# Kernel optimization log

Hardware: AMD Instinct MI355X
Metric: run time of the kernel (lower is better)

## Reference

```python
import jax, jax.numpy as jnp
import numpy as np

N, D, H, C, K, L = 50000, 256, 128, 40, 4, 2
E = 800000


def setup_inputs() -> dict:
    key = jax.random.key(0)
    ks = jax.random.split(key, 20)
    g = lambda k, s: jax.random.normal(k, s, dtype=jnp.float32) * 0.05
    z = lambda s: jnp.zeros(s, dtype=jnp.float32)
    return {
        "x": jax.random.normal(ks[0], (N, D), dtype=jnp.float32),
        "edge_index": jax.random.randint(ks[1], (2, E), 0, N, dtype=jnp.int32),
        "fc0_w": g(ks[2], (D, H)), "fc0_b": z((H,)),
        "fc1_w": g(ks[3], (H, C)), "fc1_b": z((C,)),
        "env_w": g(ks[4], (L, H, K)), "env_b": z((L, K)),
        "conv_w": g(ks[5], (L, K, 2 * H, H)),
        "q_w": g(ks[6], (H, H)), "q_b": z((H,)),
        "k_w": g(ks[7], (H, H)), "k_b": z((H,)),
        "v_w": g(ks[8], (H, H)), "v_b": z((H,)),
        "envp_w": g(ks[9], (H, K)), "envp_b": z((K,)),
        "genv_w": g(ks[10], (K, H, H)),
        "gt_w": g(ks[11], (H, H)), "gt_b": z((H,)),
    }


def _gcn_conv(h, row, col, n):
    # symmetric normalization using in-degree array (deg computed from col, as in source)
    deg = jax.ops.segment_sum(jnp.ones_like(col, dtype=h.dtype), col, num_segments=n)
    inv = jnp.where(deg > 0, 1.0 / jnp.sqrt(deg), 0.0)
    val = inv[col] * inv[row]                      # [E]
    msg = val[:, None] * h[row]                    # [E, H] gather
    return jax.ops.segment_sum(msg, col, num_segments=n)  # scatter to dst


def _canet_conv(h, row, col, env, w):
    # sum_k e_k [W_D^k * A_norm h ; W_S^k * h] via cat + per-env GEMM, residual
    hi = jnp.concatenate([_gcn_conv(h, row, col, h.shape[0]), h], axis=1)  # [N, 2H]
    out_k = jnp.einsum('nd,kdh->nkh', hi, w)       # [N, K, H]
    return jnp.einsum('nk,nkh->nh', env, out_k) + h


def _linear_transformer(h, q_w, q_b, k_w, k_b, v_w, v_b, envp_w, envp_b):
    n = h.shape[0]
    q = h @ q_w + q_b
    k = h @ k_w + k_b
    v = h @ v_w + v_b
    q = q / jnp.maximum(jnp.linalg.norm(q), 1e-12)  # fro-norm of whole matrix
    k = k / jnp.maximum(jnp.linalg.norm(k), 1e-12)
    ksum = jnp.sum(k, axis=0)                       # k^T @ ones -> [H]
    attn_norm = 1.0 + (q @ ksum)[:, None] / n       # [N,1]
    gr = (v + q @ (k.T @ v) / n) / jnp.maximum(attn_norm, 1e-12)
    return gr, gr @ envp_w + envp_b


def _forward(x, edge_index, fc0_w, fc0_b, fc1_w, fc1_b, env_w, env_b, conv_w,
             q_w, q_b, k_w, k_b, v_w, v_b, envp_w, envp_b, genv_w, gt_w, gt_b):
    row, col = edge_index[0], edge_index[1]
    h = jax.nn.relu(x @ fc0_w + fc0_b)
    for i in range(L):
        logits = h @ env_w[i] + env_b[i]            # node env encoder
        env = jax.nn.softmax(logits, axis=-1)       # eval-mode sampling
        h = jax.nn.relu(_canet_conv(h, row, col, env, conv_w[i]))
    local_logits = h @ fc1_w + fc1_b                # [N, C]
    gr, glog = _linear_transformer(h, q_w, q_b, k_w, k_b, v_w, v_b, envp_w, envp_b)
    genv = jax.nn.softmax(glog, axis=-1)            # [N, K]
    gpe = jnp.einsum('nh,khe->nke', gr, genv_w)     # per-env global transforms
    ctx = jnp.einsum('nk,nkh->nh', genv, gpe)
    gh = jax.nn.relu(ctx @ gt_w + gt_b)
    global_logits = gh @ fc1_w + fc1_b
    return 0.5 * (local_logits + global_logits)     # fused prediction


def reference(x, edge_index, fc0_w, fc0_b, fc1_w, fc1_b, env_w, env_b, conv_w,
              q_w, q_b, k_w, k_b, v_w, v_b, envp_w, envp_b, genv_w, gt_w, gt_b):
    return _forward(x, edge_index, fc0_w, fc0_b, fc1_w, fc1_b, env_w, env_b, conv_w,
                    q_w, q_b, k_w, k_b, v_w, v_b, envp_w, envp_b, genv_w, gt_w, gt_b)
```

## Files before the change

kernel.cpp:

```cpp
#include <hip/hip_runtime.h>

#define DEV __device__ __forceinline__

static constexpr int NN = 50000;
static constexpr int DD = 256;
static constexpr int HH = 128;
static constexpr int CC = 40;
static constexpr int KK = 4;
static constexpr int EE = 800000;
static constexpr int MP = 50176;
static constexpr int SKV = 196;
static constexpr int CPB = 8;
static constexpr int CSB = 391;
static constexpr int MBC = 391;

typedef __attribute__((ext_vector_type(8))) short bf16x8;
typedef __attribute__((ext_vector_type(4))) float f32x4;

DEV unsigned short f2bf(float f) {
  union { float f; unsigned int i; } c; c.f = f;
  unsigned int x = c.i;
  x += 0x7FFFu + ((x >> 16) & 1u);
  return (unsigned short)(x >> 16);
}
DEV float bfbits2f(unsigned int hi16bits) {
  union { unsigned int i; float f; } c; c.i = hi16bits; return c.f;
}

__global__ void MLEI_12970801234193_kernel(float* out, int n) {
  int i = blockIdx.x * blockDim.x + threadIdx.x;
  if (i < n) out[i] = 7.0f;
}

DEV void tc(const float* __restrict__ src, unsigned short* __restrict__ dst,
            int i, int K, int N) {
  int m = i / (K * N);
  int rem = i - m * K * N;
  int k = rem / N;
  int n = rem - k * N;
  dst[(size_t)m * K * N + (size_t)n * K + k] = f2bf(src[i]);
}

__global__ __launch_bounds__(256) void prep_kernel(
    int* __restrict__ deg, unsigned short* __restrict__ kT, unsigned short* __restrict__ vT,
    const float* __restrict__ fc0_w, unsigned short* __restrict__ Btfc0,
    const float* __restrict__ q_w, unsigned short* __restrict__ Btq,
    const float* __restrict__ k_w, unsigned short* __restrict__ Btk,
    const float* __restrict__ v_w, unsigned short* __restrict__ Btv,
    const float* __restrict__ gt_w, unsigned short* __restrict__ Btgt,
    const float* __restrict__ fc1_w, unsigned short* __restrict__ Btfc1,
    const float* __restrict__ conv_w, unsigned short* __restrict__ Btconv,
    const float* __restrict__ genv_w, unsigned short* __restrict__ Btgenv) {
  int i = blockIdx.x * 256 + threadIdx.x;
  if (i < NN) { deg[i] = 0; return; }
  i -= NN;
  const int PW = MP - NN;
  if (i < HH * PW) {
    int f = i / PW, c = i - f * PW;
    kT[(size_t)f * MP + NN + c] = 0;
    vT[(size_t)f * MP + NN + c] = 0;
    return;
  }
  i -= HH * PW;
  if (i < 32768) { tc(fc0_w, Btfc0, i, 256, 128); return; }
  i -= 32768;
  if (i < 16384) { tc(q_w, Btq, i, 128, 128); return; }
  i -= 16384;
  if (i < 16384) { tc(k_w, Btk, i, 128, 128); return; }
  i -= 16384;
  if (i < 16384) { tc(v_w, Btv, i, 128, 128); return; }
  i -= 16384;
  if (i < 16384) { tc(gt_w, Btgt, i, 128, 128); return; }
  i -= 16384;
  if (i < 5120) { tc(fc1_w, Btfc1, i, 128, 40); return; }
  i -= 5120;
  if (i < 262144) { tc(conv_w, Btconv, i, 256, 128); return; }
  i -= 262144;
  if (i < 65536) { tc(genv_w, Btgenv, i, 128, 128); }
}

__global__ __launch_bounds__(256) void mgemm_kernel(
    const float* __restrict__ A, const float* __restrict__ Aadd, int lda,
    const unsigned short* __restrict__ Bt, int K,
    int emode, float* __restrict__ out, int ldo,
    const float* __restrict__ bias, const float* __restrict__ resid, int ldr,
    const float* __restrict__ anorm, const float* __restrict__ red,
    unsigned short* __restrict__ outT,
    unsigned short* __restrict__ outBf, const float* __restrict__ rowscale,
    int M, int Nd) {
  __shared__ unsigned short As[2][128][40];
  __shared__ unsigned short Bs[2][128][40];
  const int tid = threadIdx.x, lane = tid & 63, wave = tid >> 6;
  const int quad = lane >> 4, l16 = lane & 15;
  const int wm = (wave >> 1) * 64, wn = (wave & 1) * 64;
  const int bm = blockIdx.x * 128;
  const int srow = tid >> 1, skh = (tid & 1) * 16;
  const int grow = bm + srow;
  const bool rowok = grow < M;
  const bool colok = srow < Nd;
  const int NCH = K >> 5;

  f32x4 acc[4][4];
#pragma unroll
  for (int i = 0; i < 4; ++i)
#pragma unroll
    for (int j = 0; j < 4; ++j)
#pragma unroll
      for (int r = 0; r < 4; ++r) acc[i][j][r] = 0.f;

  float vaA[16], vaB[16];
  bf16x8 bA0, bA1, bB0, bB1;

  auto LOAD = [&](int kc, float (&va)[16], bf16x8& b0, bf16x8& b1) {
    int k0 = kc << 5;
    if (rowok) {
      const float* ap = A + (size_t)grow * lda + k0 + skh;
      float4 v0 = *(const float4*)(ap + 0), v1 = *(const float4*)(ap + 4);
      float4 v2 = *(const float4*)(ap + 8), v3 = *(const float4*)(ap + 12);
      va[0] = v0.x; va[1] = v0.y; va[2] = v0.z; va[3] = v0.w;
      va[4] = v1.x; va[5] = v1.y; va[6] = v1.z; va[7] = v1.w;
      va[8] = v2.x; va[9] = v2.y; va[10] = v2.z; va[11] = v2.w;
      va[12] = v3.x; va[13] = v3.y; va[14] = v3.z; va[15] = v3.w;
      if (Aadd) {
        const float* ap2 = Aadd + (size_t)grow * lda + k0 + skh;
        float4 w0 = *(const float4*)(ap2 + 0), w1 = *(const float4*)(ap2 + 4);
        float4 w2 = *(const float4*)(ap2 + 8), w3 = *(const float4*)(ap2 + 12);
        va[0] += w0.x; va[1] += w0.y; va[2] += w0.z; va[3] += w0.w;
        va[4] += w1.x; va[5] += w1.y; va[6] += w1.z; va[7] += w1.w;
        va[8] += w2.x; va[9] += w2.y; va[10] += w2.z; va[11] += w2.w;
        va[12] += w3.x; va[13] += w3.y; va[14] += w3.z; va[15] += w3.w;
      }
    }
    if (colok) {
      const unsigned short* bp = Bt + (size_t)srow * K + k0 + skh;
      b0 = *(const bf16x8*)(bp);
      b1 = *(const bf16x8*)(bp + 8);
    } else {
#pragma unroll
      for (int z = 0; z < 8; ++z) { b0[z] = 0; b1[z] = 0; }
    }
  };

  auto STORE = [&](int buf, const float (&va)[16], const bf16x8& b0, const bf16x8& b1) {
    bf16x8 p0, p1;
    if (rowok) {
#pragma unroll
      for (int z = 0; z < 8; ++z) { p0[z] = (short)f2bf(va[z]); p1[z] = (short)f2bf(va[z + 8]); }
    } else {
#pragma unroll
      for (int z = 0; z < 8; ++z) { p0[z] = 0; p1[z] = 0; }
    }
    *(bf16x8*)&As[buf][srow][skh] = p0;
    *(bf16x8*)&As[buf][srow][skh + 8] = p1;
    *(bf16x8*)&Bs[buf][srow][skh] = b0;
    *(bf16x8*)&Bs[buf][srow][skh + 8] = b1;
  };

  auto MFMA = [&](int buf) {
    bf16x8 af[4], bfr[4];
#pragma unroll
    for (int i = 0; i < 4; ++i) af[i] = *(const bf16x8*)&As[buf][wm + i * 16 + l16][quad * 8];
#pragma unroll
    for (int j = 0; j < 4; ++j) bfr[j] = *(const bf16x8*)&Bs[buf][wn + j * 16 + l16][quad * 8];
#pragma unroll
    for (int i = 0; i < 4; ++i)
#pragma unroll
      for (int j = 0; j < 4; ++j)
        acc[i][j] = __builtin_amdgcn_mfma_f32_16x16x32_bf16(af[i], bfr[j], acc[i][j], 0, 0, 0);
  };

  LOAD(0, vaA, bA0, bA1);
  if (NCH > 1) LOAD(1, vaB, bB0, bB1);
  STORE(0, vaA, bA0, bA1);
  __syncthreads();

  for (int kc = 0; kc < NCH; kc += 2) {
    if (kc + 2 < NCH) LOAD(kc + 2, vaA, bA0, bA1);
    MFMA(0);
    if (kc + 1 < NCH) STORE(1, vaB, bB0, bB1);
    __syncthreads();
    if (kc + 1 < NCH) {
      if (kc + 3 < NCH) LOAD(kc + 3, vaB, bB0, bB1);
      MFMA(1);
      if (kc + 2 < NCH) STORE(0, vaA, bA0, bA1);
      __syncthreads();
    }
  }

  float s2 = (emode == 3) ? red[2] : 0.f;
#pragma unroll
  for (int j = 0; j < 4; ++j) {
    int col = wn + j * 16 + l16;
    if (col >= Nd) continue;
    float bv = bias ? bias[col] : 0.f;
#pragma unroll
    for (int i = 0; i < 4; ++i) {
      int row0 = bm + wm + i * 16 + quad * 4;
      if (row0 >= M) continue;
      float o[4];
#pragma unroll
      for (int r = 0; r < 4; ++r) {
        float a = acc[i][j][r];
        int row = row0 + r;
        if (emode == 0) o[r] = a + bv;
        else if (emode == 1) o[r] = fmaxf(a + bv, 0.f);
        else if (emode == 3) o[r] = (resid[(size_t)row * ldr + col] + a * s2) / anorm[row];
        else o[r] = 0.5f * a + bv;
        out[(size_t)row * ldo + col] = o[r];
      }
      if (outT) {
        ushort4 pk;
        pk.x = f2bf(o[0]); pk.y = f2bf(o[1]); pk.z = f2bf(o[2]); pk.w = f2bf(o[3]);
        *(ushort4*)&outT[(size_t)col * MP + row0] = pk;
      }
      if (outBf) {
#pragma unroll
        for (int r = 0; r < 4; ++r) {
          float rs = rowscale ? rowscale[row0 + r] : 1.f;
          outBf[(size_t)(row0 + r) * 128 + col] = f2bf(o[r] * rs);
        }
      }
    }
  }
}

__global__ __launch_bounds__(256) void mgemm_qkv_kernel(
    const float* __restrict__ A,
    const unsigned short* __restrict__ Btq, const unsigned short* __restrict__ Btk,
    const unsigned short* __restrict__ Btv,
    const float* __restrict__ q_b, const float* __restrict__ k_b,
    const float* __restrict__ v_b,
    float* __restrict__ outq, float* __restrict__ outk, float* __restrict__ outv,
    unsigned short* __restrict__ kT, unsigned short* __restrict__ vT, int M) {
  __shared__ unsigned short As[2][128][40];
  __shared__ unsigned short Bs[2][128][40];
  const int which = blockIdx.x % 3;
  const int bx = blockIdx.x / 3;
  const unsigned short* Bt = (which == 0) ? Btq : (which == 1) ? Btk : Btv;
  const float* bias = (which == 0) ? q_b : (which == 1) ? k_b : v_b;
  float* out = (which == 0) ? outq : (which == 1) ? outk : outv;
  unsigned short* outT = (which == 0) ? nullptr : (which == 1) ? kT : vT;

  const int tid = threadIdx.x, lane = tid & 63, wave = tid >> 6;
  const int quad = lane >> 4, l16 = lane & 15;
  const int wm = (wave >> 1) * 64, wn = (wave & 1) * 64;
  const int bm = bx * 128;
  const int srow = tid >> 1, skh = (tid & 1) * 16;
  const int grow = bm + srow;
  const bool rowok = grow < M;
  const int NCH = 4;

  f32x4 acc[4][4];
#pragma unroll
  for (int i = 0; i < 4; ++i)
#pragma unroll
    for (int j = 0; j < 4; ++j)
#pragma unroll
      for (int r = 0; r < 4; ++r) acc[i][j][r] = 0.f;

  float vaA[16], vaB[16];
  bf16x8 bA0, bA1, bB0, bB1;

  auto LOAD = [&](int kc, float (&va)[16], bf16x8& b0, bf16x8& b1) {
    int k0 = kc << 5;
    if (rowok) {
      const float* ap = A + (size_t)grow * 128 + k0 + skh;
      float4 v0 = *(const float4*)(ap + 0), v1 = *(const float4*)(ap + 4);
      float4 v2 = *(const float4*)(ap + 8), v3 = *(const float4*)(ap + 12);
      va[0] = v0.x; va[1] = v0.y; va[2] = v0.z; va[3] = v0.w;
      va[4] = v1.x; va[5] = v1.y; va[6] = v1.z; va[7] = v1.w;
      va[8] = v2.x; va[9] = v2.y; va[10] = v2.z; va[11] = v2.w;
      va[12] = v3.x; va[13] = v3.y; va[14] = v3.z; va[15] = v3.w;
    }
    const unsigned short* bp = Bt + (size_t)srow * 128 + k0 + skh;
    b0 = *(const bf16x8*)(bp);
    b1 = *(const bf16x8*)(bp + 8);
  };

  auto STORE = [&](int buf, const float (&va)[16], const bf16x8& b0, const bf16x8& b1) {
    bf16x8 p0, p1;
    if (rowok) {
#pragma unroll
      for (int z = 0; z < 8; ++z) { p0[z] = (short)f2bf(va[z]); p1[z] = (short)f2bf(va[z + 8]); }
    } else {
#pragma unroll
      for (int z = 0; z < 8; ++z) { p0[z] = 0; p1[z] = 0; }
    }
    *(bf16x8*)&As[buf][srow][skh] = p0;
    *(bf16x8*)&As[buf][srow][skh + 8] = p1;
    *(bf16x8*)&Bs[buf][srow][skh] = b0;
    *(bf16x8*)&Bs[buf][srow][skh + 8] = b1;
  };

  auto MFMA = [&](int buf) {
    bf16x8 af[4], bfr[4];
#pragma unroll
    for (int i = 0; i < 4; ++i) af[i] = *(const bf16x8*)&As[buf][wm + i * 16 + l16][quad * 8];
#pragma unroll
    for (int j = 0; j < 4; ++j) bfr[j] = *(const bf16x8*)&Bs[buf][wn + j * 16 + l16][quad * 8];
#pragma unroll
    for (int i = 0; i < 4; ++i)
#pragma unroll
      for (int j = 0; j < 4; ++j)
        acc[i][j] = __builtin_amdgcn_mfma_f32_16x16x32_bf16(af[i], bfr[j], acc[i][j], 0, 0, 0);
  };

  LOAD(0, vaA, bA0, bA1);
  LOAD(1, vaB, bB0, bB1);
  STORE(0, vaA, bA0, bA1);
  __syncthreads();

  for (int kc = 0; kc < NCH; kc += 2) {
    if (kc + 2 < NCH) LOAD(kc + 2, vaA, bA0, bA1);
    MFMA(0);
    if (kc + 1 < NCH) STORE(1, vaB, bB0, bB1);
    __syncthreads();
    if (kc + 1 < NCH) {
      if (kc + 3 < NCH) LOAD(kc + 3, vaB, bB0, bB1);
      MFMA(1);
      if (kc + 2 < NCH) STORE(0, vaA, bA0, bA1);
      __syncthreads();
    }
  }

#pragma unroll
  for (int j = 0; j < 4; ++j) {
    int col = wn + j * 16 + l16;
    float bv = bias[col];
#pragma unroll
    for (int i = 0; i < 4; ++i) {
      int row0 = bm + wm + i * 16 + quad * 4;
      if (row0 >= M) continue;
      float o[4];
#pragma unroll
      for (int r = 0; r < 4; ++r) {
        o[r] = acc[i][j][r] + bv;
        out[(size_t)(row0 + r) * 128 + col] = o[r];
      }
      if (outT) {
        ushort4 pk;
        pk.x = f2bf(o[0]); pk.y = f2bf(o[1]); pk.z = f2bf(o[2]); pk.w = f2bf(o[3]);
        *(ushort4*)&outT[(size_t)col * MP + row0] = pk;
      }
    }
  }
}

__global__ __launch_bounds__(256) void colstats_ktv_kernel(
    const unsigned short* __restrict__ kT, const unsigned short* __restrict__ vT,
    float* __restrict__ part,
    const float* __restrict__ q, const float* __restrict__ k,
    float* __restrict__ partK, float* __restrict__ partS, int n) {
  __shared__ unsigned short As[2][128][40];
  __shared__ unsigned short Bs[2][128][40];
  const int tid = threadIdx.x;

  if (blockIdx.x < SKV) {
    const int lane = tid & 63, wave = tid >> 6;
    const int quad = lane >> 4, l16 = lane & 15;
    const int wm = (wave >> 1) * 64, wn = (wave & 1) * 64;
    const int srow = tid >> 1, skh = (tid & 1) * 16;

    f32x4 acc[4][4];
#pragma unroll
    for (int i = 0; i < 4; ++i)
#pragma unroll
      for (int j = 0; j < 4; ++j)
#pragma unroll
        for (int r = 0; r < 4; ++r) acc[i][j][r] = 0.f;

    const int nb0 = blockIdx.x * (CPB * 32);
    bf16x8 kA0, kA1, vA0, vA1, kB0, kB1, vB0, vB1;

    auto LOAD = [&](int c, bf16x8& k0, bf16x8& k1, bf16x8& v0, bf16x8& v1) {
      int nb = nb0 + c * 32;
      const unsigned short* kp = kT + (size_t)srow * MP + nb + skh;
      k0 = *(const bf16x8*)(kp);
      k1 = *(const bf16x8*)(kp + 8);
      const unsigned short* vp = vT + (size_t)srow * MP + nb + skh;
      v0 = *(const bf16x8*)(vp);
      v1 = *(const bf16x8*)(vp + 8);
    };
    auto STORE = [&](int buf, const bf16x8& k0, const bf16x8& k1, const bf16x8& v0, const bf16x8& v1) {
      *(bf16x8*)&As[buf][srow][skh] = k0;
      *(bf16x8*)&As[buf][srow][skh + 8] = k1;
      *(bf16x8*)&Bs[buf][srow][skh] = v0;
      *(bf16x8*)&Bs[buf][srow][skh + 8] = v1;
    };
    auto MFMA = [&](int buf) {
      bf16x8 af[4], bfr[4];
#pragma unroll
      for (int i = 0; i < 4; ++i) af[i] = *(const bf16x8*)&As[buf][wm + i * 16 + l16][quad * 8];
#pragma unroll
      for (int j = 0; j < 4; ++j) bfr[j] = *(const bf16x8*)&Bs[buf][wn + j * 16 + l16][quad * 8];
#pragma unroll
      for (int i = 0; i < 4; ++i)
#pragma unroll
        for (int j = 0; j < 4; ++j)
          acc[i][j] = __builtin_amdgcn_mfma_f32_16x16x32_bf16(af[i], bfr[j], acc[i][j], 0, 0, 0);
    };

    LOAD(0, kA0, kA1, vA0, vA1);
    LOAD(1, kB0, kB1, vB0, vB1);
    STORE(0, kA0, kA1, vA0, vA1);
    __syncthreads();

    for (int c = 0; c < CPB; c += 2) {
      if (c + 2 < CPB) LOAD(c + 2, kA0, kA1, vA0, vA1);
      MFMA(0);
      if (c + 1 < CPB) STORE(1, kB0, kB1, vB0, vB1);
      __syncthreads();
      if (c + 1 < CPB) {
        if (c + 3 < CPB) LOAD(c + 3, kB0, kB1, vB0, vB1);
        MFMA(1);
        if (c + 2 < CPB) STORE(0, kA0, kA1, vA0, vA1);
        __syncthreads();
      }
    }

    float* pb = part + (size_t)blockIdx.x * 16384;
#pragma unroll
    for (int j = 0; j < 4; ++j) {
      int col = wn + j * 16 + l16;
#pragma unroll
      for (int i = 0; i < 4; ++i) {
        int row0 = wm + i * 16 + quad * 4;
        *(f32x4*)&pb[col * 128 + row0] = acc[i][j];
      }
    }
  } else {
    const int bid = blockIdx.x - SKV;
    float* sks = (float*)&As[0][0][0];
    float* ssq = sks + 256;
    float* ssk = ssq + 256;
    int ty = tid >> 7, tx = tid & 127;
    int lo = bid * 128 + ty, hi = min(n, bid * 128 + 128);
    float ks = 0.f, sq = 0.f, sk = 0.f;
    for (int r = lo; r < hi; r += 2) {
      float kv = k[(size_t)r * HH + tx];
      float qv = q[(size_t)r * HH + tx];
      ks += kv; sq += qv * qv; sk += kv * kv;
    }
    sks[ty * 128 + tx] = ks; ssq[tid] = sq; ssk[tid] = sk;
    __syncthreads();
    if (ty == 0) partK[(size_t)bid * 128 + tx] = sks[tx] + sks[128 + tx];
    for (int off = 128; off > 0; off >>= 1) {
      if (tid < off) { ssq[tid] += ssq[tid + off]; ssk[tid] += ssk[tid + off]; }
      __syncthreads();
    }
    if (tid == 0) { partS[bid * 2] = ssq[0]; partS[bid * 2 + 1] = ssk[0]; }
  }
}

__global__ void ktv_reduce_kernel(const float* __restrict__ part,
                                  unsigned short* __restrict__ Btktv) {
  int i = blockIdx.x * blockDim.x + threadIdx.x;
  if (i >= 16384) return;
  float s0 = 0.f, s1 = 0.f, s2 = 0.f, s3 = 0.f;
  int b = 0;
  for (; b + 3 < SKV; b += 4) {
    s0 += part[(size_t)b * 16384 + i];
    s1 += part[(size_t)(b + 1) * 16384 + i];
    s2 += part[(size_t)(b + 2) * 16384 + i];
    s3 += part[(size_t)(b + 3) * 16384 + i];
  }
  for (; b < SKV; ++b) s0 += part[(size_t)b * 16384 + i];
  Btktv[i] = f2bf((s0 + s1) + (s2 + s3));
}

__global__ __launch_bounds__(256) void mconv_kernel(
    const float* __restrict__ A1, const float* __restrict__ A2,
    const float* __restrict__ env, const unsigned short* __restrict__ Btc, int Kpe,
    int relu_resid, const float* __restrict__ resid, float* __restrict__ out,
    unsigned short* __restrict__ outBf, const float* __restrict__ rowscale, int M) {
  __shared__ unsigned short As[2][128][40];
  __shared__ unsigned short Bs[2][128][40];
  const int tid = threadIdx.x, lane = tid & 63, wave = tid >> 6;
  const int quad = lane >> 4, l16 = lane & 15;
  const int wm = (wave >> 1) * 64, wn = (wave & 1) * 64;
  const int bm = blockIdx.x * 128;
  const int srow = tid >> 1, skh = (tid & 1) * 16;
  const int grow = bm + srow;
  const bool rowok = grow < M;

  float ev0 = 0.f, ev1 = 0.f, ev2 = 0.f, ev3 = 0.f;
  if (rowok) {
    float4 e4 = *(const float4*)&env[(size_t)grow * 4];
    ev0 = e4.x; ev1 = e4.y; ev2 = e4.z; ev3 = e4.w;
  }

  const int npe = Kpe >> 5;
  const int NPH = npe << 2;

  f32x4 acc[4][4];
#pragma unroll
  for (int i = 0; i < 4; ++i)
#pragma unroll
    for (int j = 0; j < 4; ++j)
#pragma unroll
      for (int r = 0; r < 4; ++r) acc[i][j][r] = 0.f;

  float aC[16], aN[16];
  bf16x8 b0, b1;

  auto LOADA = [&](int kc, float (&dst)[16]) {
    int kof = kc << 5;
    const float* Asrc = A1;
    int ks = kof;
    if (A2 && kof >= 128) { Asrc = A2; ks = kof - 128; }
    if (rowok) {
      const float* ap = Asrc + (size_t)grow * 128 + ks + skh;
      float4 v0 = *(const float4*)(ap + 0), v1 = *(const float4*)(ap + 4);
      float4 v2 = *(const float4*)(ap + 8), v3 = *(const float4*)(ap + 12);
      dst[0] = v0.x; dst[1] = v0.y; dst[2] = v0.z; dst[3] = v0.w;
      dst[4] = v1.x; dst[5] = v1.y; dst[6] = v1.z; dst[7] = v1.w;
      dst[8] = v2.x; dst[9] = v2.y; dst[10] = v2.z; dst[11] = v2.w;
      dst[12] = v3.x; dst[13] = v3.y; dst[14] = v3.z; dst[15] = v3.w;
    }
  };

  auto LOADB = [&](int e, int kc) {
    const unsigned short* bp = Btc + ((size_t)e * 128 + srow) * Kpe + (kc << 5) + skh;
    b0 = *(const bf16x8*)(bp);
    b1 = *(const bf16x8*)(bp + 8);
  };

  auto STORE = [&](int buf, const float (&a)[16], float ev) {
    bf16x8 p0, p1;
    if (rowok) {
#pragma unroll
      for (int z = 0; z < 8; ++z) {
        p0[z] = (short)f2bf(a[z] * ev);
        p1[z] = (short)f2bf(a[z + 8] * ev);
      }
    } else {
#pragma unroll
      for (int z = 0; z < 8; ++z) { p0[z] = 0; p1[z] = 0; }
    }
    *(bf16x8*)&As[buf][srow][skh] = p0;
    *(bf16x8*)&As[buf][srow][skh + 8] = p1;
    *(bf16x8*)&Bs[buf][srow][skh] = b0;
    *(bf16x8*)&Bs[buf][srow][skh + 8] = b1;
  };

  auto MFMA = [&](int buf) {
    bf16x8 af[4], bfr[4];
#pragma unroll
    for (int i = 0; i < 4; ++i) af[i] = *(const bf16x8*)&As[buf][wm + i * 16 + l16][quad * 8];
#pragma unroll
    for (int j = 0; j < 4; ++j) bfr[j] = *(const bf16x8*)&Bs[buf][wn + j * 16 + l16][quad * 8];
#pragma unroll
    for (int i = 0; i < 4; ++i)
#pragma unroll
      for (int j = 0; j < 4; ++j)
        acc[i][j] = __builtin_amdgcn_mfma_f32_16x16x32_bf16(af[i], bfr[j], acc[i][j], 0, 0, 0);
  };

  LOADA(0, aC);
  LOADB(0, 0);
  if (npe > 1) LOADA(1, aN);
  STORE(0, aC, ev0);
  __syncthreads();

  for (int kc = 0; kc < npe; ++kc) {
#pragma unroll
    for (int e = 0; e < 4; ++e) {
      const int p = (kc << 2) + e;
      const int cur = e & 1;
      const bool more = (p + 1) < NPH;
      if (more) {
        LOADB((e + 1) & 3, kc + (e == 3 ? 1 : 0));
      }
      MFMA(cur);
      if (more) {
        if (e == 3) {
#pragma unroll
          for (int z = 0; z < 16; ++z) aC[z] = aN[z];
        }
        float evn = (e == 0) ? ev1 : (e == 1) ? ev2 : (e == 2) ? ev3 : ev0;
        STORE(cur ^ 1, aC, evn);
        if (e == 3 && kc + 2 < npe) LOADA(kc + 2, aN);
      }
      __syncthreads();
    }
  }

#pragma unroll
  for (int j = 0; j < 4; ++j) {
    int col = wn + j * 16 + l16;
#pragma unroll
    for (int i = 0; i < 4; ++i) {
      int row0 = bm + wm + i * 16 + quad * 4;
      if (row0 >= M) continue;
#pragma unroll
      for (int r = 0; r < 4; ++r) {
        int row = row0 + r;
        float a = acc[i][j][r];
        float o = relu_resid ? fmaxf(a + resid[(size_t)row * 128 + col], 0.f) : a;
        out[(size_t)row * 128 + col] = o;
        if (outBf) {
          float rs = rowscale ? rowscale[row] : 1.f;
          outBf[(size_t)row * 128 + col] = f2bf(o * rs);
        }
      }
    }
  }
}

__global__ void count_kernel(const int* ei, int* deg, int E) {
  int e = blockIdx.x * blockDim.x + threadIdx.x;
  if (e >= E) return;
  atomicAdd(&deg[ei[E + e]], 1);
}

__global__ __launch_bounds__(128) void scan1_kernel(const int* __restrict__ deg,
                                                    int* __restrict__ bsum, int n) {
  __shared__ int sh[128];
  int t = threadIdx.x;
  int i = blockIdx.x * 128 + t;
  sh[t] = (i < n) ? deg[i] : 0;
  __syncthreads();
  for (int off = 64; off > 0; off >>= 1) {
    if (t < off) sh[t] += sh[t + off];
    __syncthreads();
  }
  if (t == 0) bsum[blockIdx.x] = sh[0];
}

__global__ __launch_bounds__(512) void scan2_kernel(const int* __restrict__ bsum,
                                                    int* __restrict__ boff, int nb,
                                                    int* __restrict__ startN) {
  __shared__ int sh[512];
  int t = threadIdx.x;
  int v0 = (t < nb) ? bsum[t] : 0;
  sh[t] = v0;
  __syncthreads();
  for (int off = 1; off < 512; off <<= 1) {
    int v = sh[t];
    int add = (t >= off) ? sh[t - off] : 0;
    __syncthreads();
    sh[t] = v + add;
    __syncthreads();
  }
  if (t < nb) boff[t] = sh[t] - v0;
  if (t == nb - 1) *startN = sh[t];
}

__global__ __launch_bounds__(128) void scan3_kernel(const int* __restrict__ deg,
                                                    const int* __restrict__ boff,
                                                    int* __restrict__ start,
                                                    int* __restrict__ cursor,
                                                    float* __restrict__ inv, int n) {
  __shared__ int sh[128];
  int t = threadIdx.x;
  int i = blockIdx.x * 128 + t;
  int d = (i < n) ? deg[i] : 0;
  sh[t] = d;
  __syncthreads();
  for (int off = 1; off < 128; off <<= 1) {
    int v = sh[t];
    int add = (t >= off) ? sh[t - off] : 0;
    __syncthreads();
    sh[t] = v + add;
    __syncthreads();
  }
  if (i < n) {
    int p = boff[blockIdx.x] + sh[t] - d;
    start[i] = p; cursor[i] = p;
    inv[i] = (d > 0) ? rsqrtf((float)d) : 0.f;
  }
}

__global__ void fill_kernel(const int* ei, int* cursor, int* bucket, int E) {
  int e = blockIdx.x * blockDim.x + threadIdx.x;
  if (e >= E) return;
  int r = ei[e], c = ei[E + e];
  int pos = atomicAdd(&cursor[c], 1);
  bucket[pos] = r;
}

__global__ __launch_bounds__(256) void gather_env_kernel(
    const unsigned short* __restrict__ hs, const int* __restrict__ start,
    const int* __restrict__ bucket, const float* __restrict__ inv,
    const float* __restrict__ h, const float* __restrict__ w,
    const float* __restrict__ b,
    float* __restrict__ agg, float* __restrict__ env, int n) {
  int node = blockIdx.x * 4 + (threadIdx.x >> 6);
  if (node >= n) return;
  const int lane = threadIdx.x & 63;
  const int half = lane >> 5, l32 = lane & 31;
  const int f4 = l32 * 4;

  float2 hv = *(const float2*)&h[(size_t)node * 128 + 2 * lane];
  float4 w0 = *(const float4*)&w[(size_t)(2 * lane) * 4];
  float4 w1 = *(const float4*)&w[(size_t)(2 * lane + 1) * 4];
  float p0 = hv.x * w0.x + hv.y * w1.x;
  float p1 = hv.x * w0.y + hv.y * w1.y;
  float p2 = hv.x * w0.z + hv.y * w1.z;
  float p3 = hv.x * w0.w + hv.y * w1.w;

  int s0 = start[node], s1 = start[node + 1];
  float a0 = 0.f, a1 = 0.f, a2 = 0.f, a3 = 0.f;
  int j = s0 + half;
  for (; j + 2 < s1; j += 4) {
    int r0 = bucket[j], r1 = bucket[j + 2];
    uint2 u0 = *(const uint2*)&hs[(size_t)r0 * 128 + f4];
    uint2 u1 = *(const uint2*)&hs[(size_t)r1 * 128 + f4];
    a0 += bfbits2f(u0.x << 16); a1 += bfbits2f(u0.x & 0xFFFF0000u);
    a2 += bfbits2f(u0.y << 16); a3 += bfbits2f(u0.y & 0xFFFF0000u);
    a0 += bfbits2f(u1.x << 16); a1 += bfbits2f(u1.x & 0xFFFF0000u);
    a2 += bfbits2f(u1.y << 16); a3 += bfbits2f(u1.y & 0xFFFF0000u);
  }
  for (; j < s1; j += 2) {
    int r = bucket[j];
    uint2 u = *(const uint2*)&hs[(size_t)r * 128 + f4];
    a0 += bfbits2f(u.x << 16); a1 += bfbits2f(u.x & 0xFFFF0000u);
    a2 += bfbits2f(u.y << 16); a3 += bfbits2f(u.y & 0xFFFF0000u);
  }

#pragma unroll
  for (int s = 1; s <= 32; s <<= 1) {
    p0 += __shfl_xor(p0, s);
    p1 += __shfl_xor(p1, s);
    p2 += __shfl_xor(p2, s);
    p3 += __shfl_xor(p3, s);
  }

  a0 += __shfl_xor(a0, 32);
  a1 += __shfl_xor(a1, 32);
  a2 += __shfl_xor(a2, 32);
  a3 += __shfl_xor(a3, 32);
  if (half == 0) {
    float iv = inv[node];
    *(float4*)&agg[(size_t)node * 128 + f4] = make_float4(iv * a0, iv * a1, iv * a2, iv * a3);
  }
  if (lane == 0) {
    float l0 = p0 + b[0], l1 = p1 + b[1], l2 = p2 + b[2], l3 = p3 + b[3];
    float m = fmaxf(fmaxf(l0, l1), fmaxf(l2, l3));
    float e0 = __expf(l0 - m), e1 = __expf(l1 - m), e2 = __expf(l2 - m), e3 = __expf(l3 - m);
    float s = 1.f / (e0 + e1 + e2 + e3);
    *(float4*)&env[(size_t)node * 4] = make_float4(e0 * s, e1 * s, e2 * s, e3 * s);
  }
}

__global__ __launch_bounds__(256) void env_softmax_kernel(const float* __restrict__ h,
                                                          const float* __restrict__ w,
                                                          const float* __restrict__ b,
                                                          float* __restrict__ env, int M) {
  __shared__ float hsd[64][129];
  __shared__ float ws[HH * KK];
  int tid = threadIdx.x;
  int base = blockIdx.x * 64;
  for (int i = tid; i < HH * KK; i += 256) ws[i] = w[i];
  {
    int row = tid >> 2, q4 = (tid & 3) * 32;
    int g = base + row;
    if (g < M) {
      const float* hp = h + (size_t)g * HH + q4;
#pragma unroll
      for (int z = 0; z < 8; ++z) {
        float4 v = *(const float4*)(hp + z * 4);
        hsd[row][q4 + z * 4 + 0] = v.x; hsd[row][q4 + z * 4 + 1] = v.y;
        hsd[row][q4 + z * 4 + 2] = v.z; hsd[row][q4 + z * 4 + 3] = v.w;
      }
    }
  }
  __syncthreads();
  if (tid < 64 && base + tid < M) {
    float l0 = b[0], l1 = b[1], l2 = b[2], l3 = b[3];
    for (int d = 0; d < HH; ++d) {
      float hv = hsd[tid][d];
      l0 += hv * ws[d * 4 + 0]; l1 += hv * ws[d * 4 + 1];
      l2 += hv * ws[d * 4 + 2]; l3 += hv * ws[d * 4 + 3];
    }
    float m = fmaxf(fmaxf(l0, l1), fmaxf(l2, l3));
    float e0 = __expf(l0 - m), e1 = __expf(l1 - m), e2 = __expf(l2 - m), e3 = __expf(l3 - m);
    float s = 1.f / (e0 + e1 + e2 + e3);
    *(float4*)(env + (size_t)(base + tid) * KK) = make_float4(e0 * s, e1 * s, e2 * s, e3 * s);
  }
}

__global__ __launch_bounds__(256) void colstats2_kernel(
    const float* __restrict__ partK, const float* __restrict__ partS,
    float* __restrict__ ksum, float* __restrict__ red) {
  int t = threadIdx.x;
  if (t < 128) {
    float s = 0.f;
    for (int b = 0; b < CSB; ++b) s += partK[(size_t)b * 128 + t];
    ksum[t] = s;
  } else if (t == 128 || t == 129) {
    float s = 0.f;
    for (int b = 0; b < CSB; ++b) s += partS[b * 2 + (t - 128)];
    red[t - 128] = s;
  }
}

__global__ void scale_kernel(float* red, int n) {
  float nq = fmaxf(sqrtf(red[0]), 1e-12f);
  float nk = fmaxf(sqrtf(red[1]), 1e-12f);
  red[2] = 1.f / (nq * nk * (float)n);
}

__global__ __launch_bounds__(256) void anorm_kernel(const float* q, const float* ksum,
                                                    const float* red, float* anorm, int M) {
  __shared__ float ks[HH];
  for (int i = threadIdx.x; i < HH; i += blockDim.x) ks[i] = ksum[i];
  __syncthreads();
  int n = blockIdx.x * blockDim.x + threadIdx.x;
  if (n >= M) return;
  const float* qp = q + (size_t)n * HH;
  float d = 0.f;
  for (int i = 0; i < HH; ++i) d += qp[i] * ks[i];
  float a = 1.f + d * red[2];
  anorm[n] = fmaxf(a, 1e-12f);
}

extern "C" void kernel_launch(void* const* d_in, const int* in_sizes, int n_in,
                              void* d_out, int out_size, void* d_ws, size_t ws_size,
                              hipStream_t stream) {
  const float* x = (const float*)d_in[0];
  const int* ei = (const int*)d_in[1];
  const float* fc0_w = (const float*)d_in[2];
  const float* fc0_b = (const float*)d_in[3];
  const float* fc1_w = (const float*)d_in[4];
  const float* fc1_b = (const float*)d_in[5];
  const float* env_w = (const float*)d_in[6];
  const float* env_b = (const float*)d_in[7];
  const float* conv_w = (const float*)d_in[8];
  const float* q_w = (const float*)d_in[9];
  const float* q_b = (const float*)d_in[10];
  const float* k_w = (const float*)d_in[11];
  const float* k_b = (const float*)d_in[12];
  const float* v_w = (const float*)d_in[13];
  const float* v_b = (const float*)d_in[14];
  const float* envp_w = (const float*)d_in[15];
  const float* envp_b = (const float*)d_in[16];
  const float* genv_w = (const float*)d_in[17];
  const float* gt_w = (const float*)d_in[18];
  const float* gt_b = (const float*)d_in[19];
  float* out = (float*)d_out;

  const size_t NH = (size_t)NN * HH;
  float* W = (float*)d_ws;
  float* hA = W;
  float* hB = W + NH;
  float* agg = W + 2 * NH;
  float* vbuf = W + 3 * NH;
  float* gr = W + 4 * NH;
  float* env = W + 5 * NH;
  float* genv = env + (size_t)NN * KK;
  float* inv = genv + (size_t)NN * KK;
  float* anorm = inv + NN;
  float* ksum = anorm + NN;
  float* red = ksum + HH;
  int* deg = (int*)(red + 4);
  int* start = deg + NN;
  int* cursor = start + NN + 1;
  int* bucket = cursor + NN;
  int* bsum = bucket + EE;
  int* boff = bsum + CSB;
  unsigned short* wb = (unsigned short*)(((uintptr_t)(boff + CSB) + 15) & ~(uintptr_t)15);
  unsigned short* Btfc0 = wb;
  unsigned short* Btq = Btfc0 + 32768;
  unsigned short* Btk = Btq + 16384;
  unsigned short* Btv = Btk + 16384;
  unsigned short* Btgt = Btv + 16384;
  unsigned short* Btfc1 = Btgt + 16384;
  unsigned short* Btconv = Btfc1 + 5120;
  unsigned short* Btgenv = Btconv + 262144;
  unsigned short* Btktv = Btgenv + 65536;
  unsigned short* kTbf = Btktv + 16384;
  unsigned short* vTbf = kTbf + (size_t)HH * MP;
  unsigned short* hsb = vTbf + (size_t)HH * MP;
  float* part = (float*)(((uintptr_t)(hsb + NH) + 15) & ~(uintptr_t)15);
  float* partK = part + (size_t)SKV * 16384;
  float* partS = partK + (size_t)CSB * 128;

  float* q = agg;
  float* kb = hB;
  float* ctx = hB;
  float* gh = vbuf;

  dim3 b256(256);
  const int MB = MBC;
  const int PREP_TOT = NN + HH * (MP - NN) + 32768 + 4 * 16384 + 5120 + 262144 + 65536;

  prep_kernel<<<dim3((PREP_TOT + 255) / 256), b256, 0, stream>>>(
      deg, kTbf, vTbf, fc0_w, Btfc0, q_w, Btq, k_w, Btk, v_w, Btv,
      gt_w, Btgt, fc1_w, Btfc1, conv_w, Btconv, genv_w, Btgenv);

  count_kernel<<<dim3((EE + 255) / 256), b256, 0, stream>>>(ei, deg, EE);
  scan1_kernel<<<dim3(CSB), dim3(128), 0, stream>>>(deg, bsum, NN);
  scan2_kernel<<<dim3(1), dim3(512), 0, stream>>>(bsum, boff, CSB, start + NN);
  scan3_kernel<<<dim3(CSB), dim3(128), 0, stream>>>(deg, boff, start, cursor, inv, NN);
  fill_kernel<<<dim3((EE + 255) / 256), b256, 0, stream>>>(ei, cursor, bucket, EE);

  mgemm_kernel<<<dim3(MB), b256, 0, stream>>>(
      x, nullptr, DD, Btfc0, 256, 1, hA, HH, fc0_b, nullptr, 0, nullptr, nullptr,
      nullptr, hsb, inv, NN, HH);

  float* hcur = hA;
  float* hnext = hB;
  for (int l = 0; l < 2; ++l) {
    gather_env_kernel<<<dim3(NN / 4), b256, 0, stream>>>(
        hsb, start, bucket, inv, hcur, env_w + (size_t)l * HH * KK,
        env_b + (size_t)l * KK, agg, env, NN);
    mconv_kernel<<<dim3(MB), b256, 0, stream>>>(
        agg, hcur, env, Btconv + (size_t)l * 131072, 256, 1, hcur, hnext,
        (l == 0) ? hsb : nullptr, inv, NN);
    float* t = hcur; hcur = hnext; hnext = t;
  }

  mgemm_qkv_kernel<<<dim3(3 * MB), b256, 0, stream>>>(
      hcur, Btq, Btk, Btv, q_b, k_b, v_b, q, kb, vbuf, kTbf, vTbf, NN);

  colstats_ktv_kernel<<<dim3(SKV + CSB), b256, 0, stream>>>(
      kTbf, vTbf, part, q, kb, partK, partS, NN);
  colstats2_kernel<<<dim3(1), b256, 0, stream>>>(partK, partS, ksum, red);
  ktv_reduce_kernel<<<dim3(64), b256, 0, stream>>>(part, Btktv);
  scale_kernel<<<dim3(1), dim3(1), 0, stream>>>(red, NN);
  anorm_kernel<<<dim3((NN + 255) / 256), b256, 0, stream>>>(q, ksum, red, anorm, NN);

  mgemm_kernel<<<dim3(MB), b256, 0, stream>>>(
      q, nullptr, HH, Btktv, 128, 3, gr, HH, nullptr, vbuf, HH, anorm, red,
      nullptr, nullptr, nullptr, NN, HH);

  env_softmax_kernel<<<dim3((NN + 63) / 64), b256, 0, stream>>>(gr, envp_w, envp_b, genv, NN);

  mconv_kernel<<<dim3(MB), b256, 0, stream>>>(
      gr, nullptr, genv, Btgenv, 128, 0, nullptr, ctx, nullptr, nullptr, NN);

  mgemm_kernel<<<dim3(MB), b256, 0, stream>>>(
      ctx, nullptr, HH, Btgt, 128, 1, gh, HH, gt_b, nullptr, 0, nullptr, nullptr,
      nullptr, nullptr, nullptr, NN, HH);

  mgemm_kernel<<<dim3(MB), b256, 0, stream>>>(
      hcur, gh, HH, Btfc1, 128, 5, out, CC, fc1_b, nullptr, 0, nullptr, nullptr,
      nullptr, nullptr, nullptr, NN, CC);
}
```

Measured before the change: 657.3 us.

## Merge fc0 GEMM with CSR fill, fuse small reductions, widen gather loads

The fc0 GEMM and the edge-bucket fill kernel are merged into one launch, with different block ranges doing each job so they can run concurrently. The colstats2, ktv_reduce and scale kernels become a single reduce2 kernel, and the scale factor is recomputed inline wherever it is consumed. The neighbour gather now uses 16-byte loads with 16 lanes per row, covering four edges per iteration instead of two. Together these cut launch count and serial tiny kernels and raise memory-level parallelism in the gather, at the cost of more registers in the gather and a fused kernel that mixes heavy GEMM blocks with light atomic blocks.

```diff
diff --git a/kernel.cpp b/kernel.cpp
--- a/kernel.cpp
+++ b/kernel.cpp
@@ -13,6 +13,7 @@
 static constexpr int CPB = 8;
 static constexpr int CSB = 391;
 static constexpr int MBC = 391;
+static constexpr int FILLB = (EE + 255) / 256;
 
 typedef __attribute__((ext_vector_type(8))) short bf16x8;
 typedef __attribute__((ext_vector_type(4))) float f32x4;
@@ -79,7 +80,7 @@
   if (i < 65536) { tc(genv_w, Btgenv, i, 128, 128); }
 }
 
-__global__ __launch_bounds__(256) void mgemm_kernel(
+DEV void mgemm_body(
     const float* __restrict__ A, const float* __restrict__ Aadd, int lda,
     const unsigned short* __restrict__ Bt, int K,
     int emode, float* __restrict__ out, int ldo,
@@ -87,13 +88,13 @@
     const float* __restrict__ anorm, const float* __restrict__ red,
     unsigned short* __restrict__ outT,
     unsigned short* __restrict__ outBf, const float* __restrict__ rowscale,
-    int M, int Nd) {
+    int M, int Nd, int bx) {
   __shared__ unsigned short As[2][128][40];
   __shared__ unsigned short Bs[2][128][40];
   const int tid = threadIdx.x, lane = tid & 63, wave = tid >> 6;
   const int quad = lane >> 4, l16 = lane & 15;
   const int wm = (wave >> 1) * 64, wn = (wave & 1) * 64;
-  const int bm = blockIdx.x * 128;
+  const int bm = bx * 128;
   const int srow = tid >> 1, skh = (tid & 1) * 16;
   const int grow = bm + srow;
   const bool rowok = grow < M;
@@ -187,7 +188,12 @@
     }
   }
 
-  float s2 = (emode == 3) ? red[2] : 0.f;
+  float s2 = 0.f;
+  if (emode == 3) {
+    float nq = fmaxf(sqrtf(red[0]), 1e-12f);
+    float nk = fmaxf(sqrtf(red[1]), 1e-12f);
+    s2 = 1.f / (nq * nk * (float)M);
+  }
 #pragma unroll
   for (int j = 0; j < 4; ++j) {
     int col = wn + j * 16 + l16;
@@ -221,6 +227,36 @@
         }
       }
     }
+  }
+}
+
+__global__ __launch_bounds__(256) void mgemm_kernel(
+    const float* __restrict__ A, const float* __restrict__ Aadd, int lda,
+    const unsigned short* __restrict__ Bt, int K,
+    int emode, float* __restrict__ out, int ldo,
+    const float* __restrict__ bias, const float* __restrict__ resid, int ldr,
+    const float* __restrict__ anorm, const float* __restrict__ red,
+    unsigned short* __restrict__ outT,
+    unsigned short* __restrict__ outBf, const float* __restrict__ rowscale,
+    int M, int Nd) {
+  mgemm_body(A, Aadd, lda, Bt, K, emode, out, ldo, bias, resid, ldr, anorm, red,
+             outT, outBf, rowscale, M, Nd, blockIdx.x);
+}
+
+__global__ __launch_bounds__(256) void fc0_fill_kernel(
+    const float* __restrict__ x, const unsigned short* __restrict__ Btfc0,
+    const float* __restrict__ fc0_b, float* __restrict__ hA,
+    unsigned short* __restrict__ hsb, const float* __restrict__ inv,
+    const int* __restrict__ ei, int* __restrict__ cursor, int* __restrict__ bucket) {
+  if (blockIdx.x < MBC) {
+    mgemm_body(x, nullptr, DD, Btfc0, 256, 1, hA, HH, fc0_b, nullptr, 0, nullptr,
+               nullptr, nullptr, hsb, inv, NN, HH, blockIdx.x);
+  } else {
+    int e = (blockIdx.x - MBC) * 256 + threadIdx.x;
+    if (e >= EE) return;
+    int r = ei[e], c = ei[EE + e];
+    int pos = atomicAdd(&cursor[c], 1);
+    bucket[pos] = r;
   }
 }
 
@@ -452,20 +488,34 @@
   }
 }
 
-__global__ void ktv_reduce_kernel(const float* __restrict__ part,
-                                  unsigned short* __restrict__ Btktv) {
-  int i = blockIdx.x * blockDim.x + threadIdx.x;
-  if (i >= 16384) return;
-  float s0 = 0.f, s1 = 0.f, s2 = 0.f, s3 = 0.f;
-  int b = 0;
-  for (; b + 3 < SKV; b += 4) {
-    s0 += part[(size_t)b * 16384 + i];
-    s1 += part[(size_t)(b + 1) * 16384 + i];
-    s2 += part[(size_t)(b + 2) * 16384 + i];
-    s3 += part[(size_t)(b + 3) * 16384 + i];
-  }
-  for (; b < SKV; ++b) s0 += part[(size_t)b * 16384 + i];
-  Btktv[i] = f2bf((s0 + s1) + (s2 + s3));
+__global__ __launch_bounds__(256) void reduce2_kernel(
+    const float* __restrict__ partK, const float* __restrict__ partS,
+    float* __restrict__ ksum, float* __restrict__ red,
+    const float* __restrict__ part, unsigned short* __restrict__ Btktv) {
+  int t = threadIdx.x;
+  if (blockIdx.x == 0) {
+    if (t < 128) {
+      float s = 0.f;
+      for (int b = 0; b < CSB; ++b) s += partK[(size_t)b * 128 + t];
+      ksum[t] = s;
+    } else if (t == 128 || t == 129) {
+      float s = 0.f;
+      for (int b = 0; b < CSB; ++b) s += partS[b * 2 + (t - 128)];
+      red[t - 128] = s;
+    }
+  } else {
+    int i = (blockIdx.x - 1) * 256 + t;
+    float s0 = 0.f, s1 = 0.f, s2 = 0.f, s3 = 0.f;
+    int b = 0;
+    for (; b + 3 < SKV; b += 4) {
+      s0 += part[(size_t)b * 16384 + i];
+      s1 += part[(size_t)(b + 1) * 16384 + i];
+      s2 += part[(size_t)(b + 2) * 16384 + i];
+      s3 += part[(size_t)(b + 3) * 16384 + i];
+    }
+    for (; b < SKV; ++b) s0 += part[(size_t)b * 16384 + i];
+    Btktv[i] = f2bf((s0 + s1) + (s2 + s3));
+  }
 }
 
 __global__ __launch_bounds__(256) void mconv_kernel(
@@ -671,14 +721,6 @@
   }
 }
 
-__global__ void fill_kernel(const int* ei, int* cursor, int* bucket, int E) {
-  int e = blockIdx.x * blockDim.x + threadIdx.x;
-  if (e >= E) return;
-  int r = ei[e], c = ei[E + e];
-  int pos = atomicAdd(&cursor[c], 1);
-  bucket[pos] = r;
-}
-
 __global__ __launch_bounds__(256) void gather_env_kernel(
     const unsigned short* __restrict__ hs, const int* __restrict__ start,
     const int* __restrict__ bucket, const float* __restrict__ inv,
@@ -688,8 +730,8 @@
   int node = blockIdx.x * 4 + (threadIdx.x >> 6);
   if (node >= n) return;
   const int lane = threadIdx.x & 63;
-  const int half = lane >> 5, l32 = lane & 31;
-  const int f4 = l32 * 4;
+  const int quarter = lane >> 4, l16 = lane & 15;
+  const int f8 = l16 * 8;
 
   float2 hv = *(const float2*)&h[(size_t)node * 128 + 2 * lane];
   float4 w0 = *(const float4*)&w[(size_t)(2 * lane) * 4];
@@ -701,21 +743,28 @@
 
   int s0 = start[node], s1 = start[node + 1];
   float a0 = 0.f, a1 = 0.f, a2 = 0.f, a3 = 0.f;
-  int j = s0 + half;
-  for (; j + 2 < s1; j += 4) {
-    int r0 = bucket[j], r1 = bucket[j + 2];
-    uint2 u0 = *(const uint2*)&hs[(size_t)r0 * 128 + f4];
-    uint2 u1 = *(const uint2*)&hs[(size_t)r1 * 128 + f4];
+  float a4 = 0.f, a5 = 0.f, a6 = 0.f, a7 = 0.f;
+  int j = s0 + quarter;
+  for (; j + 4 < s1; j += 8) {
+    int r0 = bucket[j], r1 = bucket[j + 4];
+    uint4 u0 = *(const uint4*)&hs[(size_t)r0 * 128 + f8];
+    uint4 u1 = *(const uint4*)&hs[(size_t)r1 * 128 + f8];
     a0 += bfbits2f(u0.x << 16); a1 += bfbits2f(u0.x & 0xFFFF0000u);
     a2 += bfbits2f(u0.y << 16); a3 += bfbits2f(u0.y & 0xFFFF0000u);
+    a4 += bfbits2f(u0.z << 16); a5 += bfbits2f(u0.z & 0xFFFF0000u);
+    a6 += bfbits2f(u0.w << 16); a7 += bfbits2f(u0.w & 0xFFFF0000u);
     a0 += bfbits2f(u1.x << 16); a1 += bfbits2f(u1.x & 0xFFFF0000u);
     a2 += bfbits2f(u1.y << 16); a3 += bfbits2f(u1.y & 0xFFFF0000u);
-  }
-  for (; j < s1; j += 2) {
+    a4 += bfbits2f(u1.z << 16); a5 += bfbits2f(u1.z & 0xFFFF0000u);
+    a6 += bfbits2f(u1.w << 16); a7 += bfbits2f(u1.w & 0xFFFF0000u);
+  }
+  for (; j < s1; j += 4) {
     int r = bucket[j];
-    uint2 u = *(const uint2*)&hs[(size_t)r * 128 + f4];
+    uint4 u = *(const uint4*)&hs[(size_t)r * 128 + f8];
     a0 += bfbits2f(u.x << 16); a1 += bfbits2f(u.x & 0xFFFF0000u);
     a2 += bfbits2f(u.y << 16); a3 += bfbits2f(u.y & 0xFFFF0000u);
+    a4 += bfbits2f(u.z << 16); a5 += bfbits2f(u.z & 0xFFFF0000u);
+    a6 += bfbits2f(u.w << 16); a7 += bfbits2f(u.w & 0xFFFF0000u);
   }
 
 #pragma unroll
@@ -726,13 +775,19 @@
     p3 += __shfl_xor(p3, s);
   }
 
-  a0 += __shfl_xor(a0, 32);
-  a1 += __shfl_xor(a1, 32);
-  a2 += __shfl_xor(a2, 32);
-  a3 += __shfl_xor(a3, 32);
-  if (half == 0) {
+  a0 += __shfl_xor(a0, 16); a1 += __shfl_xor(a1, 16);
+  a2 += __shfl_xor(a2, 16); a3 += __shfl_xor(a3, 16);
+  a4 += __shfl_xor(a4, 16); a5 += __shfl_xor(a5, 16);
+  a6 += __shfl_xor(a6, 16); a7 += __shfl_xor(a7, 16);
+  a0 += __shfl_xor(a0, 32); a1 += __shfl_xor(a1, 32);
+  a2 += __shfl_xor(a2, 32); a3 += __shfl_xor(a3, 32);
+  a4 += __shfl_xor(a4, 32); a5 += __shfl_xor(a5, 32);
+  a6 += __shfl_xor(a6, 32); a7 += __shfl_xor(a7, 32);
+
+  if (lane < 16) {
     float iv = inv[node];
-    *(float4*)&agg[(size_t)node * 128 + f4] = make_float4(iv * a0, iv * a1, iv * a2, iv * a3);
+    *(float4*)&agg[(size_t)node * 128 + f8] = make_float4(iv * a0, iv * a1, iv * a2, iv * a3);
+    *(float4*)&agg[(size_t)node * 128 + f8 + 4] = make_float4(iv * a4, iv * a5, iv * a6, iv * a7);
   }
   if (lane == 0) {
     float l0 = p0 + b[0], l1 = p1 + b[1], l2 = p2 + b[2], l3 = p3 + b[3];
@@ -780,27 +835,6 @@
   }
 }
 
-__global__ __launch_bounds__(256) void colstats2_kernel(
-    const float* __restrict__ partK, const float* __restrict__ partS,
-    float* __restrict__ ksum, float* __restrict__ red) {
-  int t = threadIdx.x;
-  if (t < 128) {
-    float s = 0.f;
-    for (int b = 0; b < CSB; ++b) s += partK[(size_t)b * 128 + t];
-    ksum[t] = s;
-  } else if (t == 128 || t == 129) {
-    float s = 0.f;
-    for (int b = 0; b < CSB; ++b) s += partS[b * 2 + (t - 128)];
-    red[t - 128] = s;
-  }
-}
-
-__global__ void scale_kernel(float* red, int n) {
-  float nq = fmaxf(sqrtf(red[0]), 1e-12f);
-  float nk = fmaxf(sqrtf(red[1]), 1e-12f);
-  red[2] = 1.f / (nq * nk * (float)n);
-}
-
 __global__ __launch_bounds__(256) void anorm_kernel(const float* q, const float* ksum,
                                                     const float* red, float* anorm, int M) {
   __shared__ float ks[HH];
@@ -808,10 +842,13 @@
   __syncthreads();
   int n = blockIdx.x * blockDim.x + threadIdx.x;
   if (n >= M) return;
+  float nq = fmaxf(sqrtf(red[0]), 1e-12f);
+  float nk = fmaxf(sqrtf(red[1]), 1e-12f);
+  float s2 = 1.f / (nq * nk * (float)M);
   const float* qp = q + (size_t)n * HH;
   float d = 0.f;
   for (int i = 0; i < HH; ++i) d += qp[i] * ks[i];
-  float a = 1.f + d * red[2];
+  float a = 1.f + d * s2;
   anorm[n] = fmaxf(a, 1e-12f);
 }
 
@@ -893,11 +930,9 @@
   scan1_kernel<<<dim3(CSB), dim3(128), 0, stream>>>(deg, bsum, NN);
   scan2_kernel<<<dim3(1), dim3(512), 0, stream>>>(bsum, boff, CSB, start + NN);
   scan3_kernel<<<dim3(CSB), dim3(128), 0, stream>>>(deg, boff, start, cursor, inv, NN);
-  fill_kernel<<<dim3((EE + 255) / 256), b256, 0, stream>>>(ei, cursor, bucket, EE);
-
-  mgemm_kernel<<<dim3(MB), b256, 0, stream>>>(
-      x, nullptr, DD, Btfc0, 256, 1, hA, HH, fc0_b, nullptr, 0, nullptr, nullptr,
-      nullptr, hsb, inv, NN, HH);
+
+  fc0_fill_kernel<<<dim3(MBC + FILLB), b256, 0, stream>>>(
+      x, Btfc0, fc0_b, hA, hsb, inv, ei, cursor, bucket);
 
   float* hcur = hA;
   float* hnext = hB;
@@ -916,9 +951,7 @@
 
   colstats_ktv_kernel<<<dim3(SKV + CSB), b256, 0, stream>>>(
       kTbf, vTbf, part, q, kb, partK, partS, NN);
-  colstats2_kernel<<<dim3(1), b256, 0, stream>>>(partK, partS, ksum, red);
-  ktv_reduce_kernel<<<dim3(64), b256, 0, stream>>>(part, Btktv);
-  scale_kernel<<<dim3(1), dim3(1), 0, stream>>>(red, NN);
+  reduce2_kernel<<<dim3(65), b256, 0, stream>>>(partK, partS, ksum, red, part, Btktv);
   anorm_kernel<<<dim3((NN + 255) / 256), b256, 0, stream>>>(q, ksum, red, anorm, NN);
 
   mgemm_kernel<<<dim3(MB), b256, 0, stream>>>(
```

After: 612.7 us. 1.07x faster.
